# Kernel tuning notes

Measured on AMD Instinct MI355X. Metric: run time of the kernel, lower is better.

Reference implementation:

```python
import jax, jax.numpy as jnp
import numpy as np

D_MODEL = 512
N_HEADS = 8
Q_SEQ_LEN = 1024
KV_SEQ_LEN = 1024
N_MODES = 64
D_HEAD = D_MODEL // N_HEADS

# FEDformer frequency_modes (deterministic/lowest branch): lowest n_modes freqs
Q_MODES = np.arange(min(N_MODES, Q_SEQ_LEN // 2))
KV_MODES = np.arange(min(N_MODES, KV_SEQ_LEN // 2))


def setup_inputs() -> dict:
    key = jax.random.key(0)
    kq, kk, kv, kwr, kwi = jax.random.split(key, 5)
    B = 8
    scale = 1.0 / (D_MODEL * D_MODEL)
    return {
        "query": jax.random.normal(kq, (B, N_HEADS, Q_SEQ_LEN, D_HEAD), jnp.float32),
        "key": jax.random.normal(kk, (B, N_HEADS, KV_SEQ_LEN, D_HEAD), jnp.float32),
        "value": jax.random.normal(kv, (B, N_HEADS, KV_SEQ_LEN, D_HEAD), jnp.float32),
        "weights_re": scale * jax.random.uniform(kwr, (N_HEADS, D_HEAD, D_HEAD, len(Q_MODES)), jnp.float32),
        "weights_im": scale * jax.random.uniform(kwi, (N_HEADS, D_HEAD, D_HEAD, len(Q_MODES)), jnp.float32),
    }


def reference(query, key, value, weights_re, weights_im):
    # value is accepted but unused by the original forward (FEA-f variant).
    B, H, L, D = query.shape
    q_modes = jnp.asarray(Q_MODES)
    kv_modes = jnp.asarray(KV_MODES)

    # [B,H,D,L] -> rfft along time -> gather selected frequency modes
    q_fft = jnp.fft.rfft(jnp.swapaxes(query, -2, -1), axis=-1)   # [B,H,D,L//2+1]
    k_fft = jnp.fft.rfft(jnp.swapaxes(key, -2, -1), axis=-1)     # [B,H,D,Lk//2+1]
    q_fft = jnp.take(q_fft, q_modes, axis=-1)                    # [B,H,D,Mq]
    k_fft = jnp.take(k_fft, kv_modes, axis=-1)                   # [B,H,D,Mk]

    # complex attention in frequency domain (no conjugation, as in torch einsum)
    scores_fft = jnp.einsum('bhdq,bhdk->bhqk', q_fft, k_fft)
    attn_fft = jnp.tanh(scores_fft)
    context_fft = jnp.einsum('bhqk,bhdk->bhdq', attn_fft, k_fft)  # [B,H,D,Mq]

    w = (weights_re + 1j * weights_im).astype(jnp.complex64)      # [H,D,D,Mq]
    context_fft = jnp.einsum('bhiq,hijq->bhjq', context_fft, w)   # [B,H,D,Mq]

    # scatter modes back into full rfft spectrum, then irfft
    out_fft = jnp.zeros((B, H, D, L // 2 + 1), jnp.complex64)
    out_fft = out_fft.at[..., q_modes].set(context_fft)
    d_model = H * D
    context = jnp.fft.irfft(out_fft / d_model / d_model, n=L, axis=-1)  # [B,H,D,L]
    return context
```

## Files before the change

### kernel.cpp

```cpp
#include <hip/hip_runtime.h>
#include <hip/hip_bf16.h>
#include <cmath>

#define BATCH 8
#define NH 8
#define BH 64
#define SEQ 1024
#define DH 64
#define NM 64

#define P_PLANE 4096
#define P_FLOATS (2*4*64*2*4096)
#define C1R_OFF  P_FLOATS
#define C1I_OFF  (C1R_OFF + 64*64*64)
#define C2_OFF   (C1I_OFF + 64*64*64)

__global__ __launch_bounds__(256) void k_dft(const float* __restrict__ q,
                                             const float* __restrict__ k,
                                             float* __restrict__ P) {
  const int bid = blockIdx.x;
  const int bh = bid & 63;
  const int inp = (bid >> 6) & 1;
  const int tq = bid >> 7;
  const float* x = (inp ? k : q) + (size_t)bh * (SEQ * DH);

  __shared__ float xs[64][64];
  const int tid = threadIdx.x;
  const int m = tid >> 2;
  const int d0 = (tid & 3) * 16;

  float accr[16] = {0.f}, acci[16] = {0.f};

  const float phs = (float)m * (1.0f / 512.0f);
  const float stepc = cospif(phs);
  const float steps = -sinpif(phs);

  for (int ch = 0; ch < 4; ++ch) {
    const int t0g = tq * 256 + ch * 64;
    const float4* src = reinterpret_cast<const float4*>(x + (size_t)t0g * DH);
    float4* dst = reinterpret_cast<float4*>(&xs[0][0]);
#pragma unroll
    for (int i = 0; i < 4; ++i) dst[tid + i * 256] = src[tid + i * 256];
    __syncthreads();

    const int p0 = (m * t0g) & 1023;
    const float ph0 = (float)p0 * (1.0f / 512.0f);
    float wr = cospif(ph0);
    float wi = -sinpif(ph0);

#pragma unroll 4
    for (int t = 0; t < 64; ++t) {
      float4 a = *reinterpret_cast<const float4*>(&xs[t][d0]);
      float4 b = *reinterpret_cast<const float4*>(&xs[t][d0 + 4]);
      float4 c = *reinterpret_cast<const float4*>(&xs[t][d0 + 8]);
      float4 e = *reinterpret_cast<const float4*>(&xs[t][d0 + 12]);
      float xv[16] = {a.x, a.y, a.z, a.w, b.x, b.y, b.z, b.w,
                      c.x, c.y, c.z, c.w, e.x, e.y, e.z, e.w};
#pragma unroll
      for (int di = 0; di < 16; ++di) {
        accr[di] = fmaf(wr, xv[di], accr[di]);
        acci[di] = fmaf(wi, xv[di], acci[di]);
      }
      float nr = wr * stepc - wi * steps;
      float ni = wr * steps + wi * stepc;
      wr = nr; wi = ni;
    }
    __syncthreads();
  }

  const size_t base = ((((size_t)inp * 4 + tq) * 64 + bh) * 2) * P_PLANE;
  float* pr = P + base + (size_t)m * 64 + d0;
  float* pi = P + base + P_PLANE + (size_t)m * 64 + d0;
#pragma unroll
  for (int i = 0; i < 4; ++i) {
    *reinterpret_cast<float4*>(pr + i * 4) =
        make_float4(accr[i * 4], accr[i * 4 + 1], accr[i * 4 + 2], accr[i * 4 + 3]);
    *reinterpret_cast<float4*>(pi + i * 4) =
        make_float4(acci[i * 4], acci[i * 4 + 1], acci[i * 4 + 2], acci[i * 4 + 3]);
  }
}

__device__ __forceinline__ void ctanh_f(float x, float y, float& rr, float& ri) {
  float a = 2.0f * x, b = 2.0f * y;
  if (fabsf(a) > 20.0f) {
    rr = (a > 0.0f) ? 1.0f : -1.0f;
    ri = 0.0f;
  } else {
    float ea = expf(a), ena = expf(-a);
    float sb, cb;
    sincosf(b, &sb, &cb);
    float den = 0.5f * (ea + ena) + cb;
    rr = 0.5f * (ea - ena) / den;
    ri = sb / den;
  }
}

__global__ __launch_bounds__(256) void k_mid_a(const float* __restrict__ P,
                                               float* __restrict__ C1r,
                                               float* __restrict__ C1i) {
  __shared__ float Kr[64][67], Ki[64][67];
  __shared__ float Qr[16][67], Qi[16][67];
  __shared__ float Ar[16][67], Ai[16][67];
  __shared__ float C1rs[64][17], C1is[64][17];

  const int tid = threadIdx.x;
  const int bh = blockIdx.x >> 2;
  const int qq = blockIdx.x & 3;

  size_t pq[4], pk[4];
#pragma unroll
  for (int t = 0; t < 4; ++t) {
    pq[t] = (((size_t)(0 * 4 + t) * 64 + bh) * 2) * P_PLANE;
    pk[t] = (((size_t)(1 * 4 + t) * 64 + bh) * 2) * P_PLANE;
  }

  for (int idx = tid; idx < 4096; idx += 256) {
    int kk = idx >> 6, dd = idx & 63;
    float r = 0.f, im = 0.f;
#pragma unroll
    for (int t = 0; t < 4; ++t) {
      r += P[pk[t] + idx];
      im += P[pk[t] + P_PLANE + idx];
    }
    Kr[kk][dd] = r; Ki[kk][dd] = im;
  }
  for (int idx = tid; idx < 1024; idx += 256) {
    int qi2 = idx >> 6, dd = idx & 63;
    int mm = qq * 16 + qi2;
    float r = 0.f, im = 0.f;
#pragma unroll
    for (int t = 0; t < 4; ++t) {
      r += P[pq[t] + mm * 64 + dd];
      im += P[pq[t] + P_PLANE + mm * 64 + dd];
    }
    Qr[qi2][dd] = r; Qi[qi2][dd] = im;
  }
  __syncthreads();

  {
    const int q = tid >> 4, k0 = (tid & 15) * 4;
    float sr[4] = {0.f}, si[4] = {0.f};
    for (int d = 0; d < 64; ++d) {
      float qr = Qr[q][d], qi = Qi[q][d];
#pragma unroll
      for (int j = 0; j < 4; ++j) {
        float kr = Kr[k0 + j][d], ki = Ki[k0 + j][d];
        sr[j] = fmaf(qr, kr, sr[j]); sr[j] = fmaf(-qi, ki, sr[j]);
        si[j] = fmaf(qr, ki, si[j]); si[j] = fmaf(qi, kr, si[j]);
      }
    }
#pragma unroll
    for (int j = 0; j < 4; ++j) {
      float rr, ri;
      ctanh_f(sr[j], si[j], rr, ri);
      Ar[q][k0 + j] = rr;
      Ai[q][k0 + j] = ri;
    }
  }
  __syncthreads();

  {
    const int q = tid >> 4, d0 = (tid & 15) * 4;
    float cr[4] = {0.f}, ci[4] = {0.f};
    for (int kk = 0; kk < 64; ++kk) {
      float ar = Ar[q][kk], ai = Ai[q][kk];
#pragma unroll
      for (int j = 0; j < 4; ++j) {
        float kr = Kr[kk][d0 + j], ki = Ki[kk][d0 + j];
        cr[j] = fmaf(ar, kr, cr[j]); cr[j] = fmaf(-ai, ki, cr[j]);
        ci[j] = fmaf(ar, ki, ci[j]); ci[j] = fmaf(ai, kr, ci[j]);
      }
    }
#pragma unroll
    for (int j = 0; j < 4; ++j) { C1rs[d0 + j][q] = cr[j]; C1is[d0 + j][q] = ci[j]; }
  }
  __syncthreads();

  for (int idx = tid; idx < 1024; idx += 256) {
    int i = idx >> 4, ql = idx & 15;
    size_t o = ((size_t)bh * 64 + i) * 64 + qq * 16 + ql;
    C1r[o] = C1rs[i][ql];
    C1i[o] = C1is[i][ql];
  }
}

__global__ __launch_bounds__(64) void k_mid_b(const float* __restrict__ C1r,
                                              const float* __restrict__ C1i,
                                              const float* __restrict__ wre,
                                              const float* __restrict__ wim,
                                              float* __restrict__ C2) {
  const int bid = blockIdx.x;
  const int j = bid & 63;
  const int h = (bid >> 6) & 7;
  const int bq = bid >> 9;
  const int lane = threadIdx.x;

  float ar[2] = {0.f, 0.f}, ai[2] = {0.f, 0.f};
  for (int i = 0; i < 64; ++i) {
    size_t wo = (((size_t)h * 64 + i) * 64 + j) * 64 + lane;
    float wr = wre[wo], wi = wim[wo];
#pragma unroll
    for (int bb = 0; bb < 2; ++bb) {
      int bh = (bq * 2 + bb) * 8 + h;
      size_t co = ((size_t)bh * 64 + i) * 64 + lane;
      float c1r = C1r[co], c1i = C1i[co];
      ar[bb] = fmaf(c1r, wr, ar[bb]); ar[bb] = fmaf(-c1i, wi, ar[bb]);
      ai[bb] = fmaf(c1r, wi, ai[bb]); ai[bb] = fmaf(c1i, wr, ai[bb]);
    }
  }
#pragma unroll
  for (int bb = 0; bb < 2; ++bb) {
    int bh = (bq * 2 + bb) * 8 + h;
    *reinterpret_cast<float2*>(&C2[(((size_t)bh * 64 + j) * 64 + lane) * 2]) =
        make_float2(ar[bb], ai[bb]);
  }
}

__global__ __launch_bounds__(256) void k_idft(const float* __restrict__ C2,
                                              float* __restrict__ out) {
  __shared__ float Cr[64][68], Ci[64][68];
  const int tid = threadIdx.x;
  const int bh = blockIdx.x >> 4;
  const int tc = blockIdx.x & 15;
  const float s = 1.0f / (512.0f * 512.0f * 1024.0f);

  for (int idx = tid; idx < 4096; idx += 256) {
    int j = idx >> 6, m = idx & 63;
    float f = (m == 0) ? s : 2.0f * s;
    float2 c = *reinterpret_cast<const float2*>(&C2[(((size_t)bh * 64 + j) * 64 + m) * 2]);
    Cr[m][j] = f * c.x;
    Ci[m][j] = f * c.y;
  }
  __syncthreads();

  const int tg = tid & 31, jg = tid >> 5;
  const int t0 = tc * 64 + tg * 2, j0 = jg * 8;

  float sc[2], ss[2], wc[2], wsn[2];
#pragma unroll
  for (int kk = 0; kk < 2; ++kk) {
    float ph = (float)((t0 + kk) & 1023) * (1.0f / 512.0f);
    sc[kk] = cospif(ph);
    ss[kk] = sinpif(ph);
    wc[kk] = 1.0f;
    wsn[kk] = 0.0f;
  }

  float acc[2][8] = {{0.f}};
  for (int m = 0; m < 64; ++m) {
    float4 c0 = *reinterpret_cast<const float4*>(&Cr[m][j0]);
    float4 c1 = *reinterpret_cast<const float4*>(&Cr[m][j0 + 4]);
    float4 e0 = *reinterpret_cast<const float4*>(&Ci[m][j0]);
    float4 e1 = *reinterpret_cast<const float4*>(&Ci[m][j0 + 4]);
    float crv[8] = {c0.x, c0.y, c0.z, c0.w, c1.x, c1.y, c1.z, c1.w};
    float civ[8] = {e0.x, e0.y, e0.z, e0.w, e1.x, e1.y, e1.z, e1.w};
#pragma unroll
    for (int kk = 0; kk < 2; ++kk) {
      float cw = wc[kk], sw = wsn[kk];
#pragma unroll
      for (int jj = 0; jj < 8; ++jj) {
        acc[kk][jj] = fmaf(crv[jj], cw, acc[kk][jj]);
        acc[kk][jj] = fmaf(-civ[jj], sw, acc[kk][jj]);
      }
      float nr = cw * sc[kk] - sw * ss[kk];
      float ni = cw * ss[kk] + sw * sc[kk];
      wc[kk] = nr; wsn[kk] = ni;
    }
  }

#pragma unroll
  for (int jj = 0; jj < 8; ++jj) {
    *reinterpret_cast<float2*>(&out[(size_t)bh * 65536 + (size_t)(j0 + jj) * 1024 + t0]) =
        make_float2(acc[0][jj], acc[1][jj]);
  }
}

extern "C" void kernel_launch(void* const* d_in, const int* in_sizes, int n_in,
                              void* d_out, int out_size, void* d_ws, size_t ws_size,
                              hipStream_t stream) {
  const float* q   = (const float*)d_in[0];
  const float* k   = (const float*)d_in[1];
  const float* wre = (const float*)d_in[3];
  const float* wim = (const float*)d_in[4];
  float* out = (float*)d_out;
  float* ws  = (float*)d_ws;

  float* P   = ws;
  float* C1r = ws + C1R_OFF;
  float* C1i = ws + C1I_OFF;
  float* C2  = ws + C2_OFF;

  k_dft  <<<512,  256, 0, stream>>>(q, k, P);
  k_mid_a<<<256,  256, 0, stream>>>(P, C1r, C1i);
  k_mid_b<<<2048,  64, 0, stream>>>(C1r, C1i, wre, wim, C2);
  k_idft <<<1024, 256, 0, stream>>>(C2, out);
}
```

Baseline: 178.1 us.

## Retile DFT, vectorize mid-stage LDS reads, interleave C1 complex, widen iDFT tiles

The DFT kernel now gives each thread 2 modes by 8 channels instead of 1 mode by 16 channels, which changes how LDS reads are reused against twiddle work. In k_mid_a the LDS rows are padded to 68 so float4 reads are aligned, and the score loop is reorganised to use float4 loads with strided key assignment. C1 is stored as interleaved complex so k_mid_b can issue one float2 load per element, with pointers hoisted and the loop unrolled. The iDFT computes 4 time points per thread and uses float4 stores on half as many blocks, which raises register pressure and lowers block count.

```diff
diff --git a/kernel.cpp b/kernel.cpp
--- a/kernel.cpp
+++ b/kernel.cpp
@@ -11,9 +11,8 @@
 
 #define P_PLANE 4096
 #define P_FLOATS (2*4*64*2*4096)
-#define C1R_OFF  P_FLOATS
-#define C1I_OFF  (C1R_OFF + 64*64*64)
-#define C2_OFF   (C1I_OFF + 64*64*64)
+#define C1C_OFF  P_FLOATS
+#define C2_OFF   (C1C_OFF + 64*64*64*2)
 
 __global__ __launch_bounds__(256) void k_dft(const float* __restrict__ q,
                                              const float* __restrict__ k,
@@ -26,14 +25,19 @@
 
   __shared__ float xs[64][64];
   const int tid = threadIdx.x;
-  const int m = tid >> 2;
-  const int d0 = (tid & 3) * 16;
-
-  float accr[16] = {0.f}, acci[16] = {0.f};
-
-  const float phs = (float)m * (1.0f / 512.0f);
-  const float stepc = cospif(phs);
-  const float steps = -sinpif(phs);
+  const int mg = tid >> 3;
+  const int dg = tid & 7;
+  const int m0 = mg * 2, d0 = dg * 8;
+
+  float accr[2][8] = {{0.f}}, acci[2][8] = {{0.f}};
+
+  float stepc[2], steps[2];
+#pragma unroll
+  for (int mi = 0; mi < 2; ++mi) {
+    float ph = (float)(m0 + mi) * (1.0f / 512.0f);
+    stepc[mi] = cospif(ph);
+    steps[mi] = -sinpif(ph);
+  }
 
   for (int ch = 0; ch < 4; ++ch) {
     const int t0g = tq * 256 + ch * 64;
@@ -43,40 +47,49 @@
     for (int i = 0; i < 4; ++i) dst[tid + i * 256] = src[tid + i * 256];
     __syncthreads();
 
-    const int p0 = (m * t0g) & 1023;
-    const float ph0 = (float)p0 * (1.0f / 512.0f);
-    float wr = cospif(ph0);
-    float wi = -sinpif(ph0);
+    float wr[2], wi[2];
+#pragma unroll
+    for (int mi = 0; mi < 2; ++mi) {
+      int p0 = ((m0 + mi) * t0g) & 1023;
+      float ph = (float)p0 * (1.0f / 512.0f);
+      wr[mi] = cospif(ph);
+      wi[mi] = -sinpif(ph);
+    }
 
 #pragma unroll 4
     for (int t = 0; t < 64; ++t) {
       float4 a = *reinterpret_cast<const float4*>(&xs[t][d0]);
       float4 b = *reinterpret_cast<const float4*>(&xs[t][d0 + 4]);
-      float4 c = *reinterpret_cast<const float4*>(&xs[t][d0 + 8]);
-      float4 e = *reinterpret_cast<const float4*>(&xs[t][d0 + 12]);
-      float xv[16] = {a.x, a.y, a.z, a.w, b.x, b.y, b.z, b.w,
-                      c.x, c.y, c.z, c.w, e.x, e.y, e.z, e.w};
-#pragma unroll
-      for (int di = 0; di < 16; ++di) {
-        accr[di] = fmaf(wr, xv[di], accr[di]);
-        acci[di] = fmaf(wi, xv[di], acci[di]);
+      float xv[8] = {a.x, a.y, a.z, a.w, b.x, b.y, b.z, b.w};
+#pragma unroll
+      for (int mi = 0; mi < 2; ++mi) {
+        float cwr = wr[mi], cwi = wi[mi];
+#pragma unroll
+        for (int di = 0; di < 8; ++di) {
+          accr[mi][di] = fmaf(cwr, xv[di], accr[mi][di]);
+          acci[mi][di] = fmaf(cwi, xv[di], acci[mi][di]);
+        }
+        float nr = cwr * stepc[mi] - cwi * steps[mi];
+        float ni = cwr * steps[mi] + cwi * stepc[mi];
+        wr[mi] = nr; wi[mi] = ni;
       }
-      float nr = wr * stepc - wi * steps;
-      float ni = wr * steps + wi * stepc;
-      wr = nr; wi = ni;
     }
     __syncthreads();
   }
 
-  const size_t base = ((((size_t)inp * 4 + tq) * 64 + bh) * 2) * P_PLANE;
-  float* pr = P + base + (size_t)m * 64 + d0;
-  float* pi = P + base + P_PLANE + (size_t)m * 64 + d0;
-#pragma unroll
-  for (int i = 0; i < 4; ++i) {
-    *reinterpret_cast<float4*>(pr + i * 4) =
-        make_float4(accr[i * 4], accr[i * 4 + 1], accr[i * 4 + 2], accr[i * 4 + 3]);
-    *reinterpret_cast<float4*>(pi + i * 4) =
-        make_float4(acci[i * 4], acci[i * 4 + 1], acci[i * 4 + 2], acci[i * 4 + 3]);
+  const size_t base = (((size_t)inp * 4 + tq) * 64 + bh) * 2 * P_PLANE;
+#pragma unroll
+  for (int mi = 0; mi < 2; ++mi) {
+    float* pr = P + base + (size_t)(m0 + mi) * 64 + d0;
+    float* pi = P + base + P_PLANE + (size_t)(m0 + mi) * 64 + d0;
+    *reinterpret_cast<float4*>(pr) =
+        make_float4(accr[mi][0], accr[mi][1], accr[mi][2], accr[mi][3]);
+    *reinterpret_cast<float4*>(pr + 4) =
+        make_float4(accr[mi][4], accr[mi][5], accr[mi][6], accr[mi][7]);
+    *reinterpret_cast<float4*>(pi) =
+        make_float4(acci[mi][0], acci[mi][1], acci[mi][2], acci[mi][3]);
+    *reinterpret_cast<float4*>(pi + 4) =
+        make_float4(acci[mi][4], acci[mi][5], acci[mi][6], acci[mi][7]);
   }
 }
 
@@ -96,11 +109,10 @@
 }
 
 __global__ __launch_bounds__(256) void k_mid_a(const float* __restrict__ P,
-                                               float* __restrict__ C1r,
-                                               float* __restrict__ C1i) {
-  __shared__ float Kr[64][67], Ki[64][67];
-  __shared__ float Qr[16][67], Qi[16][67];
-  __shared__ float Ar[16][67], Ai[16][67];
+                                               float* __restrict__ C1c) {
+  __shared__ float Kr[64][68], Ki[64][68];
+  __shared__ float Qr[16][68], Qi[16][68];
+  __shared__ float Ar[16][68], Ai[16][68];
   __shared__ float C1rs[64][17], C1is[64][17];
 
   const int tid = threadIdx.x;
@@ -138,23 +150,34 @@
   __syncthreads();
 
   {
-    const int q = tid >> 4, k0 = (tid & 15) * 4;
+    const int q = tid >> 4, k0 = tid & 15;
     float sr[4] = {0.f}, si[4] = {0.f};
-    for (int d = 0; d < 64; ++d) {
-      float qr = Qr[q][d], qi = Qi[q][d];
+    for (int d = 0; d < 64; d += 4) {
+      const float4 qr = *reinterpret_cast<const float4*>(&Qr[q][d]);
+      const float4 qi = *reinterpret_cast<const float4*>(&Qi[q][d]);
 #pragma unroll
       for (int j = 0; j < 4; ++j) {
-        float kr = Kr[k0 + j][d], ki = Ki[k0 + j][d];
-        sr[j] = fmaf(qr, kr, sr[j]); sr[j] = fmaf(-qi, ki, sr[j]);
-        si[j] = fmaf(qr, ki, si[j]); si[j] = fmaf(qi, kr, si[j]);
+        const int kk = k0 + 16 * j;
+        const float4 kr = *reinterpret_cast<const float4*>(&Kr[kk][d]);
+        const float4 ki = *reinterpret_cast<const float4*>(&Ki[kk][d]);
+        float s0 = sr[j], s1 = si[j];
+        s0 = fmaf(qr.x, kr.x, s0); s0 = fmaf(-qi.x, ki.x, s0);
+        s1 = fmaf(qr.x, ki.x, s1); s1 = fmaf(qi.x, kr.x, s1);
+        s0 = fmaf(qr.y, kr.y, s0); s0 = fmaf(-qi.y, ki.y, s0);
+        s1 = fmaf(qr.y, ki.y, s1); s1 = fmaf(qi.y, kr.y, s1);
+        s0 = fmaf(qr.z, kr.z, s0); s0 = fmaf(-qi.z, ki.z, s0);
+        s1 = fmaf(qr.z, ki.z, s1); s1 = fmaf(qi.z, kr.z, s1);
+        s0 = fmaf(qr.w, kr.w, s0); s0 = fmaf(-qi.w, ki.w, s0);
+        s1 = fmaf(qr.w, ki.w, s1); s1 = fmaf(qi.w, kr.w, s1);
+        sr[j] = s0; si[j] = s1;
       }
     }
 #pragma unroll
     for (int j = 0; j < 4; ++j) {
       float rr, ri;
       ctanh_f(sr[j], si[j], rr, ri);
-      Ar[q][k0 + j] = rr;
-      Ai[q][k0 + j] = ri;
+      Ar[q][k0 + 16 * j] = rr;
+      Ai[q][k0 + 16 * j] = ri;
     }
   }
   __syncthreads();
@@ -164,28 +187,30 @@
     float cr[4] = {0.f}, ci[4] = {0.f};
     for (int kk = 0; kk < 64; ++kk) {
       float ar = Ar[q][kk], ai = Ai[q][kk];
-#pragma unroll
-      for (int j = 0; j < 4; ++j) {
-        float kr = Kr[kk][d0 + j], ki = Ki[kk][d0 + j];
-        cr[j] = fmaf(ar, kr, cr[j]); cr[j] = fmaf(-ai, ki, cr[j]);
-        ci[j] = fmaf(ar, ki, ci[j]); ci[j] = fmaf(ai, kr, ci[j]);
-      }
-    }
-#pragma unroll
-    for (int j = 0; j < 4; ++j) { C1rs[d0 + j][q] = cr[j]; C1is[d0 + j][q] = ci[j]; }
+      const float4 kr = *reinterpret_cast<const float4*>(&Kr[kk][d0]);
+      const float4 ki = *reinterpret_cast<const float4*>(&Ki[kk][d0]);
+      cr[0] = fmaf(ar, kr.x, cr[0]); cr[0] = fmaf(-ai, ki.x, cr[0]);
+      ci[0] = fmaf(ar, ki.x, ci[0]); ci[0] = fmaf(ai, kr.x, ci[0]);
+      cr[1] = fmaf(ar, kr.y, cr[1]); cr[1] = fmaf(-ai, ki.y, cr[1]);
+      ci[1] = fmaf(ar, ki.y, ci[1]); ci[1] = fmaf(ai, kr.y, ci[1]);
+      cr[2] = fmaf(ar, kr.z, cr[2]); cr[2] = fmaf(-ai, ki.z, cr[2]);
+      ci[2] = fmaf(ar, ki.z, ci[2]); ci[2] = fmaf(ai, kr.z, ci[2]);
+      cr[3] = fmaf(ar, kr.w, cr[3]); cr[3] = fmaf(-ai, ki.w, cr[3]);
+      ci[3] = fmaf(ar, ki.w, ci[3]); ci[3] = fmaf(ai, kr.w, ci[3]);
+    }
+#pragma unroll
+    for (int j = 0; j < 4; ++j) { C1rs[d0 + j][tid >> 4] = cr[j]; C1is[d0 + j][tid >> 4] = ci[j]; }
   }
   __syncthreads();
 
   for (int idx = tid; idx < 1024; idx += 256) {
     int i = idx >> 4, ql = idx & 15;
-    size_t o = ((size_t)bh * 64 + i) * 64 + qq * 16 + ql;
-    C1r[o] = C1rs[i][ql];
-    C1i[o] = C1is[i][ql];
-  }
-}
-
-__global__ __launch_bounds__(64) void k_mid_b(const float* __restrict__ C1r,
-                                              const float* __restrict__ C1i,
+    size_t o = (((size_t)bh * 64 + i) * 64 + qq * 16 + ql) * 2;
+    *reinterpret_cast<float2*>(&C1c[o]) = make_float2(C1rs[i][ql], C1is[i][ql]);
+  }
+}
+
+__global__ __launch_bounds__(64) void k_mid_b(const float* __restrict__ C1c,
                                               const float* __restrict__ wre,
                                               const float* __restrict__ wim,
                                               float* __restrict__ C2) {
@@ -195,33 +220,35 @@
   const int bq = bid >> 9;
   const int lane = threadIdx.x;
 
-  float ar[2] = {0.f, 0.f}, ai[2] = {0.f, 0.f};
+  const int bh0 = (bq * 2 + 0) * 8 + h;
+  const int bh1 = (bq * 2 + 1) * 8 + h;
+  const float2* c1a = reinterpret_cast<const float2*>(C1c) + (size_t)bh0 * 4096 + lane;
+  const float2* c1b = reinterpret_cast<const float2*>(C1c) + (size_t)bh1 * 4096 + lane;
+  const float* wrp = wre + ((size_t)h * 4096 + j) * 64 + lane;
+  const float* wip = wim + ((size_t)h * 4096 + j) * 64 + lane;
+
+  float ar0 = 0.f, ai0 = 0.f, ar1 = 0.f, ai1 = 0.f;
+#pragma unroll 8
   for (int i = 0; i < 64; ++i) {
-    size_t wo = (((size_t)h * 64 + i) * 64 + j) * 64 + lane;
-    float wr = wre[wo], wi = wim[wo];
-#pragma unroll
-    for (int bb = 0; bb < 2; ++bb) {
-      int bh = (bq * 2 + bb) * 8 + h;
-      size_t co = ((size_t)bh * 64 + i) * 64 + lane;
-      float c1r = C1r[co], c1i = C1i[co];
-      ar[bb] = fmaf(c1r, wr, ar[bb]); ar[bb] = fmaf(-c1i, wi, ar[bb]);
-      ai[bb] = fmaf(c1r, wi, ai[bb]); ai[bb] = fmaf(c1i, wr, ai[bb]);
-    }
-  }
-#pragma unroll
-  for (int bb = 0; bb < 2; ++bb) {
-    int bh = (bq * 2 + bb) * 8 + h;
-    *reinterpret_cast<float2*>(&C2[(((size_t)bh * 64 + j) * 64 + lane) * 2]) =
-        make_float2(ar[bb], ai[bb]);
-  }
+    float wr = wrp[(size_t)i * 4096];
+    float wi = wip[(size_t)i * 4096];
+    float2 ca = c1a[(size_t)i * 64];
+    float2 cb = c1b[(size_t)i * 64];
+    ar0 = fmaf(ca.x, wr, ar0); ar0 = fmaf(-ca.y, wi, ar0);
+    ai0 = fmaf(ca.x, wi, ai0); ai0 = fmaf(ca.y, wr, ai0);
+    ar1 = fmaf(cb.x, wr, ar1); ar1 = fmaf(-cb.y, wi, ar1);
+    ai1 = fmaf(cb.x, wi, ai1); ai1 = fmaf(cb.y, wr, ai1);
+  }
+  *reinterpret_cast<float2*>(&C2[(((size_t)bh0 * 64 + j) * 64 + lane) * 2]) = make_float2(ar0, ai0);
+  *reinterpret_cast<float2*>(&C2[(((size_t)bh1 * 64 + j) * 64 + lane) * 2]) = make_float2(ar1, ai1);
 }
 
 __global__ __launch_bounds__(256) void k_idft(const float* __restrict__ C2,
                                               float* __restrict__ out) {
   __shared__ float Cr[64][68], Ci[64][68];
   const int tid = threadIdx.x;
-  const int bh = blockIdx.x >> 4;
-  const int tc = blockIdx.x & 15;
+  const int bh = blockIdx.x >> 3;
+  const int tc = blockIdx.x & 7;
   const float s = 1.0f / (512.0f * 512.0f * 1024.0f);
 
   for (int idx = tid; idx < 4096; idx += 256) {
@@ -234,11 +261,11 @@
   __syncthreads();
 
   const int tg = tid & 31, jg = tid >> 5;
-  const int t0 = tc * 64 + tg * 2, j0 = jg * 8;
-
-  float sc[2], ss[2], wc[2], wsn[2];
-#pragma unroll
-  for (int kk = 0; kk < 2; ++kk) {
+  const int t0 = tc * 128 + tg * 4, j0 = jg * 8;
+
+  float sc[4], ss[4], wc[4], wsn[4];
+#pragma unroll
+  for (int kk = 0; kk < 4; ++kk) {
     float ph = (float)((t0 + kk) & 1023) * (1.0f / 512.0f);
     sc[kk] = cospif(ph);
     ss[kk] = sinpif(ph);
@@ -246,7 +273,7 @@
     wsn[kk] = 0.0f;
   }
 
-  float acc[2][8] = {{0.f}};
+  float acc[4][8] = {{0.f}};
   for (int m = 0; m < 64; ++m) {
     float4 c0 = *reinterpret_cast<const float4*>(&Cr[m][j0]);
     float4 c1 = *reinterpret_cast<const float4*>(&Cr[m][j0 + 4]);
@@ -255,7 +282,7 @@
     float crv[8] = {c0.x, c0.y, c0.z, c0.w, c1.x, c1.y, c1.z, c1.w};
     float civ[8] = {e0.x, e0.y, e0.z, e0.w, e1.x, e1.y, e1.z, e1.w};
 #pragma unroll
-    for (int kk = 0; kk < 2; ++kk) {
+    for (int kk = 0; kk < 4; ++kk) {
       float cw = wc[kk], sw = wsn[kk];
 #pragma unroll
       for (int jj = 0; jj < 8; ++jj) {
@@ -270,8 +297,8 @@
 
 #pragma unroll
   for (int jj = 0; jj < 8; ++jj) {
-    *reinterpret_cast<float2*>(&out[(size_t)bh * 65536 + (size_t)(j0 + jj) * 1024 + t0]) =
-        make_float2(acc[0][jj], acc[1][jj]);
+    *reinterpret_cast<float4*>(&out[(size_t)bh * 65536 + (size_t)(j0 + jj) * 1024 + t0]) =
+        make_float4(acc[0][jj], acc[1][jj], acc[2][jj], acc[3][jj]);
   }
 }
 
@@ -286,12 +313,11 @@
   float* ws  = (float*)d_ws;
 
   float* P   = ws;
-  float* C1r = ws + C1R_OFF;
-  float* C1i = ws + C1I_OFF;
+  float* C1c = ws + C1C_OFF;
   float* C2  = ws + C2_OFF;
 
   k_dft  <<<512,  256, 0, stream>>>(q, k, P);
-  k_mid_a<<<256,  256, 0, stream>>>(P, C1r, C1i);
-  k_mid_b<<<2048,  64, 0, stream>>>(C1r, C1i, wre, wim, C2);
-  k_idft <<<1024, 256, 0, stream>>>(C2, out);
-}
+  k_mid_a<<<256,  256, 0, stream>>>(P, C1c);
+  k_mid_b<<<2048,  64, 0, stream>>>(C1c, wre, wim, C2);
+  k_idft <<<512,  256, 0, stream>>>(C2, out);
+}
```

Result: no change. 175.4 us (-1.5%).
